# Kernel optimization log

Hardware: AMD Instinct MI355X
Metric: run time of the kernel (lower is better)

## Reference

```python
import jax, jax.numpy as jnp
import numpy as np
import math

B = 32; N = 512000; D = 64; NENT = 100000; NEDGE = 1000000; NREL = 200
K_SOURCE = 100; K_MIN = 50; K_MAX = 1000; L_INFL = 4; A_SLOPE = 1.0
TEMP = 1.0; LAM_NOISE = 1.0; COS_EPS = 1e-8


def compute_topk(l):
    # sigmoid schedule for layer-dependent Top-K (python ints, trace-time)
    if l < L_INFL:
        s = 1.0 / (1.0 + math.exp(-A_SLOPE * (l - L_INFL / 2)))
        return int(K_SOURCE + (K_MAX - K_SOURCE) * s)
    s = 1.0 / (1.0 + math.exp(-A_SLOPE * (l - 3 * L_INFL / 2)))
    return int(K_MIN + (K_MAX - K_MIN) * (1.0 - s))


def setup_inputs():
    key = jax.random.key(0)
    k = jax.random.split(key, 14)
    i = jnp.arange(N)
    b = i % B                     # batches interleaved -> every batch has diff nodes
    e = (i // B) * 6 + b          # unique entity per (batch, node), max < NENT
    nodes = jnp.stack([b, e], axis=1)
    return {
        "hidden": jax.random.normal(k[0], (N, D), jnp.float32),
        "nodes": nodes,
        "scores": jax.random.uniform(k[1], (N,), jnp.float32) + 0.1,
        "h0": jax.random.normal(k[2], (1, N, D), jnp.float32),
        "alpha": jax.random.normal(k[3], (NEDGE, 1), jnp.float32),
        "hidden_q": jax.random.normal(k[4], (B, D), jnp.float32),
        "q_rel": jax.random.randint(k[5], (B,), 0, 2 * NREL + 1),
        "edges": jax.random.randint(k[6], (NEDGE, 6), 0, N),
        "old_nodes_new_idx": jnp.arange(N // 2),
        "batch_size": B,
        "message": jax.random.normal(k[7], (NEDGE, D), jnp.float32),
        "obj": jax.random.randint(k[8], (NEDGE,), 0, N),
        "alpha_temp": jax.random.normal(k[9], (NEDGE, 1), jnp.float32),
        "l": 2,
        "noise": jax.random.normal(k[10], (N, 3), jnp.float32),
        "mlp_w1": jax.random.normal(k[11], (2 * D, D), jnp.float32) * 0.05,
        "mlp_b1": jnp.zeros((D,), jnp.float32),
        "mlp_w2": jax.random.normal(k[12], (D, D), jnp.float32) * 0.05,
        "mlp_b2": jnp.zeros((D,), jnp.float32),
        "rel_embed": jax.random.normal(k[13], (2 * NREL + 1, D), jnp.float32) * 0.05,
        "expert_emb": jax.random.normal(jax.random.fold_in(key, 1), (3, D), jnp.float32),
        "w_n": jax.random.normal(jax.random.fold_in(key, 2), (D,), jnp.float32) * 0.05,
    }


def _dense_topk_mult(vals, bidx, eidx, diff, K, B_):
    # scatter per-diff-node values into dense [B, n_ent], softmax over entities,
    # top-K hard mask, straight-through multiplier (hard - sg(p) + p) on diff nodes.
    neg = jnp.float32(-jnp.inf)
    dense = jnp.full((B_, NENT), neg, jnp.float32).at[bidx, eidx].set(jnp.where(diff, vals, neg))
    probs = jax.nn.softmax(dense, axis=1)
    _, idx = jax.lax.top_k(probs, K)
    hard = jnp.zeros((B_, NENT), bool).at[jnp.arange(B_)[:, None], idx].set(True)
    p = probs[bidx, eidx]
    h = hard[bidx, eidx].astype(jnp.float32)
    return jnp.where(diff, h - jax.lax.stop_gradient(p) + p, 1.0)


def _forward(hidden, scores, h0, hidden_q, alpha_temp, mlp_w1, mlp_b1, mlp_w2, mlp_b2,
             rel_embed, expert_emb, w_n, nodes, q_rel, edges, old_nodes_new_idx,
             batch_size, noise, l):
    bidx = nodes[:, 0]
    eidx = nodes[:, 1]
    # ---- noisy gate over 3 pruning experts ----
    q_rel_e = rel_embed[q_rel]                                   # [B, D]
    ctx_in = jnp.concatenate([hidden_q[bidx], q_rel_e[bidx]], axis=-1)  # [N, 2D]
    ctx = jax.nn.relu(ctx_in @ mlp_w1 + mlp_b1) @ mlp_w2 + mlp_b2       # [N, D]
    escore = ctx @ expert_emb.T                                  # [N, 3]
    nscale = jax.nn.softplus(ctx @ w_n)[:, None]                 # [N, 1]
    escore = escore + LAM_NOISE * noise * nscale
    weights = jax.nn.softmax(escore / TEMP, axis=-1)             # [N, 3]
    importance = weights.sum(0) / weights.sum()                  # [3], sums to 1
    w = importance  # num_pruning_experts=3: topk over all 3 + renorm is identity

    diff = jnp.ones((N,), bool).at[old_nodes_new_idx].set(False)
    K_l = compute_topk(l)

    # expert 0: score-based pruner
    m0 = _dense_topk_mult(scores, bidx, eidx, diff, K_l, batch_size)

    # expert 1: cosine-similarity pruner (hidden vs query relation embedding)
    qn = q_rel_e[bidx]
    num = (hidden * qn).sum(-1)
    den = jnp.maximum(jnp.linalg.norm(hidden, axis=-1), COS_EPS) * \
          jnp.maximum(jnp.linalg.norm(qn, axis=-1), COS_EPS)
    m1 = _dense_topk_mult(num / den, bidx, eidx, diff, K_l, batch_size)

    # expert 2: alpha pruner -- segment-max of edge attention onto target nodes,
    # softmax over the global node dim, top-K among new nodes only.
    obj_e = edges[:, 5]
    mx = jax.ops.segment_max(alpha_temp[:, 0], obj_e, num_segments=N)
    node_probs = jax.nn.softmax(mx / TEMP)
    masked = jnp.where(diff, node_probs, -1.0)   # probs >= 0, so topk lands on diff
    _, top_i = jax.lax.top_k(masked, K_l)
    hard2 = jnp.zeros((N,), bool).at[top_i].set(True)
    m2 = jnp.where(diff, hard2.astype(jnp.float32) - jax.lax.stop_gradient(node_probs) + node_probs, 1.0)

    # ---- combine: each expert returns the full node set with diff rows rescaled,
    # and the hashed node-id lookup is the identity permutation here, so the
    # index_add combine reduces to a weighted sum of multipliers. ----
    wm = w[0] * m0 + w[1] * m1 + w[2] * m2                        # [N]
    hidden_c = hidden * wm[:, None]
    scores_c = scores * wm
    h0_c = h0 * wm[None, :, None]

    cv = jnp.std(weights, ddof=1) / (weights.mean() + 1e-5)       # torch unbiased std
    L_imp = cv ** 2
    return hidden_c, scores_c, h0_c, L_imp


def reference(hidden, nodes, scores, h0, alpha, hidden_q, q_rel, edges,
              old_nodes_new_idx, batch_size, message, obj, alpha_temp, l, noise,
              mlp_w1, mlp_b1, mlp_w2, mlp_b2, rel_embed, expert_emb, w_n):
    # alpha / message / obj are passed through in the original but unused in the
    # computed path; the final scores!=0 row filter is replaced by keeping the
    # full (zero-preserving) arrays to stay jit-compatible.
    return _forward(hidden, scores, h0, hidden_q, alpha_temp, mlp_w1, mlp_b1,
                    mlp_w2, mlp_b2, rel_embed, expert_emb, w_n, nodes, q_rel,
                    edges, old_nodes_new_idx, batch_size, noise, l)
```

## Files before the change

kernel.cpp:

```cpp
#include <hip/hip_runtime.h>
#include <stdint.h>
#include <math.h>

#define DD 64
#define K_SOURCE_C 100
#define K_MIN_C 50
#define K_MAX_C 1000
#define L_INFL_C 4
#define A_SLOPE_C 1.0
#define COS_EPS_C 1e-8f
#define NSEL_MAX 65
#define NBINS 8192

__device__ __forceinline__ uint32_t f2mono(float f) {
    uint32_t u = __float_as_uint(f);
    return (u & 0x80000000u) ? ~u : (u | 0x80000000u);
}

__constant__ int c_shifts[5] = {51, 38, 25, 12, 0};
__constant__ int c_nbits[5]  = {13, 13, 13, 13, 12};

__global__ void init_kernel(uint32_t* mx, uint8_t* diff, int* cnt, double* sums,
                            int* Kp, const int* l_ptr, int N, int B) {
    int i = blockIdx.x * blockDim.x + threadIdx.x;
    if (i < N) { mx[i] = 0u; diff[i] = 1; }
    if (i < B) cnt[i] = 0;
    if (i < 4) sums[i] = 0.0;
    if (i == 0) {
        double l = (double)(*l_ptr);
        int K;
        if (l < (double)L_INFL_C) {
            double s = 1.0 / (1.0 + exp(-A_SLOPE_C * (l - L_INFL_C / 2.0)));
            K = (int)(K_SOURCE_C + (K_MAX_C - K_SOURCE_C) * s);
        } else {
            double s = 1.0 / (1.0 + exp(-A_SLOPE_C * (l - 3.0 * L_INFL_C / 2.0)));
            K = (int)(K_MIN_C + (K_MAX_C - K_MIN_C) * (1.0 - s));
        }
        *Kp = K;
    }
}

__global__ void zero_ghist_kernel(uint32_t* ghist, int total) {
    int i = blockIdx.x * blockDim.x + threadIdx.x;
    if (i < total) ghist[i] = 0;
}

__global__ void state_init_kernel(uint64_t* prefix, uint32_t* Krs, uint32_t* done,
                                  const int* Kp, int nsel) {
    int s = threadIdx.x;
    if (s < nsel) { prefix[s] = 0ull; Krs[s] = (uint32_t)(*Kp); done[s] = 0u; }
}

__global__ void diff_kernel(uint8_t* diff, const int* old_idx, int n_old, int N) {
    int j = blockIdx.x * blockDim.x + threadIdx.x;
    if (j < n_old) { int idx = old_idx[j]; if (idx >= 0 && idx < N) diff[idx] = 0; }
}

__global__ void ctx_kernel(const float* hidden_q, const int* q_rel, const float* rel_embed,
                           const float* w1, const float* b1, const float* w2, const float* b2,
                           const float* expert_emb, const float* w_n,
                           float* escore, float* nscale, float* qvec, float* qnorm, int B) {
    int b = blockIdx.x, t = threadIdx.x;
    __shared__ float cin[2 * DD];
    __shared__ float h1s[DD];
    int q = q_rel[b];
    float qv = rel_embed[(size_t)q * DD + t];
    qvec[b * DD + t] = qv;
    cin[t] = hidden_q[b * DD + t];
    cin[DD + t] = qv;
    __syncthreads();
    float acc = b1[t];
    for (int j = 0; j < 2 * DD; j++) acc += cin[j] * w1[j * DD + t];
    h1s[t] = fmaxf(acc, 0.f);
    __syncthreads();
    float c = b2[t];
    for (int j = 0; j < DD; j++) c += h1s[j] * w2[j * DD + t];
    float e0 = c * expert_emb[0 * DD + t];
    float e1 = c * expert_emb[1 * DD + t];
    float e2 = c * expert_emb[2 * DD + t];
    float wn = c * w_n[t];
    float qq = qv * qv;
    for (int m = 32; m >= 1; m >>= 1) {
        e0 += __shfl_xor(e0, m); e1 += __shfl_xor(e1, m); e2 += __shfl_xor(e2, m);
        wn += __shfl_xor(wn, m); qq += __shfl_xor(qq, m);
    }
    if (t == 0) {
        escore[b * 3 + 0] = e0; escore[b * 3 + 1] = e1; escore[b * 3 + 2] = e2;
        nscale[b] = fmaxf(wn, 0.f) + log1pf(expf(-fabsf(wn)));
        qnorm[b] = fmaxf(sqrtf(qq), COS_EPS_C);
    }
}

__global__ void weights_kernel(const int* nodes, const float* noise, const float* escore,
                               const float* nscale, double* sums, int N, int B) {
    int i = blockIdx.x * blockDim.x + threadIdx.x;
    double s0 = 0, s1 = 0, s2 = 0, sq = 0;
    if (i < N) {
        int b = nodes[2 * i];
        if (b >= 0 && b < B) {
            float ns = nscale[b];
            float e0 = escore[b * 3 + 0] + noise[3 * i + 0] * ns;
            float e1 = escore[b * 3 + 1] + noise[3 * i + 1] * ns;
            float e2 = escore[b * 3 + 2] + noise[3 * i + 2] * ns;
            float m = fmaxf(e0, fmaxf(e1, e2));
            float x0 = expf(e0 - m), x1 = expf(e1 - m), x2 = expf(e2 - m);
            float s = x0 + x1 + x2;
            x0 /= s; x1 /= s; x2 /= s;
            s0 = x0; s1 = x1; s2 = x2;
            sq = (double)x0 * x0 + (double)x1 * x1 + (double)x2 * x2;
        }
    }
    for (int m = 32; m >= 1; m >>= 1) {
        s0 += __shfl_xor(s0, m); s1 += __shfl_xor(s1, m);
        s2 += __shfl_xor(s2, m); sq += __shfl_xor(sq, m);
    }
    __shared__ double red[4][4];
    int wid = threadIdx.x >> 6, lane = threadIdx.x & 63;
    if (lane == 0) { red[wid][0] = s0; red[wid][1] = s1; red[wid][2] = s2; red[wid][3] = sq; }
    __syncthreads();
    if (threadIdx.x == 0) {
        int nw = blockDim.x >> 6;
        double a0 = 0, a1 = 0, a2 = 0, a3 = 0;
        for (int w = 0; w < nw; w++) { a0 += red[w][0]; a1 += red[w][1]; a2 += red[w][2]; a3 += red[w][3]; }
        atomicAdd(&sums[0], a0); atomicAdd(&sums[1], a1);
        atomicAdd(&sums[2], a2); atomicAdd(&sums[3], a3);
    }
}

__global__ void stats_kernel(const double* sums, float* wvec, float* out_L, int N) {
    double c0 = sums[0], c1 = sums[1], c2 = sums[2], S2 = sums[3];
    double tot = c0 + c1 + c2;
    wvec[0] = (float)(c0 / tot); wvec[1] = (float)(c1 / tot); wvec[2] = (float)(c2 / tot);
    double n = 3.0 * (double)N;
    double mean = tot / n;
    double var = (S2 - tot * tot / n) / (n - 1.0);
    if (var < 0) var = 0;
    double cv = sqrt(var) / (mean + 1e-5);
    *out_L = (float)(cv * cv);
}

__global__ void cos_kernel(const float* hidden, const int* nodes, const float* qvec,
                           const float* qnorm, float* cosvals, int N, int B) {
    int t = threadIdx.x;
    int node = blockIdx.x * 16 + (t >> 4);
    int sub = t & 15;
    if (node >= N) return;
    int b = nodes[2 * node];
    float4 h4 = *(const float4*)(hidden + (size_t)node * DD + sub * 4);
    float num = 0.f;
    if (b >= 0 && b < B) {
        float4 q4 = *(const float4*)(qvec + b * DD + sub * 4);
        num = h4.x * q4.x + h4.y * q4.y + h4.z * q4.z + h4.w * q4.w;
    }
    float hs = h4.x * h4.x + h4.y * h4.y + h4.z * h4.z + h4.w * h4.w;
    for (int m = 8; m >= 1; m >>= 1) { num += __shfl_xor(num, m); hs += __shfl_xor(hs, m); }
    if (sub == 0) {
        float qn = (b >= 0 && b < B) ? qnorm[b] : COS_EPS_C;
        cosvals[node] = num / (fmaxf(sqrtf(hs), COS_EPS_C) * qn);
    }
}

__global__ void segmax_kernel(const int* edges, const float* alpha_temp, uint32_t* mx,
                              int NE, int N) {
    int e = blockIdx.x * blockDim.x + threadIdx.x;
    if (e < NE) {
        int o = edges[(size_t)e * 6 + 5];
        if (o >= 0 && o < N) atomicMax(&mx[o], f2mono(alpha_temp[e]));
    }
}

__global__ void compact_kernel(const int* nodes, const uint8_t* diff, const float* scores,
                               const float* cosvals, uint64_t* keys0, uint64_t* keys1,
                               int* cnt, int N, int B, int CAP) {
    __shared__ int lcnt[64];
    __shared__ int lbase[64];
    int t = threadIdx.x;
    if (t < B) lcnt[t] = 0;
    __syncthreads();
    int i = blockIdx.x * blockDim.x + t;
    int b = -1, loc = 0;
    if (i < N && diff[i]) {
        int bb = nodes[2 * i];
        if (bb >= 0 && bb < B) { b = bb; loc = atomicAdd(&lcnt[b], 1); }
    }
    __syncthreads();
    if (t < B) lbase[t] = lcnt[t] ? atomicAdd(&cnt[t], lcnt[t]) : 0;
    __syncthreads();
    if (b >= 0) {
        int pos = lbase[b] + loc;
        if (pos < CAP) {
            int ei = nodes[2 * i + 1];
            uint64_t tb = (uint64_t)(0xFFFFFFFFu - (uint32_t)ei);
            keys0[(size_t)b * CAP + pos] = ((uint64_t)f2mono(scores[i]) << 32) | tb;
            keys1[(size_t)b * CAP + pos] = ((uint64_t)f2mono(cosvals[i]) << 32) | tb;
        }
    }
}

__global__ __launch_bounds__(1024)
void hist_kernel(const uint64_t* keys0, const uint64_t* keys1, const int* cnt,
                 const uint8_t* diff, const uint32_t* mx,
                 const uint64_t* prefix, const uint32_t* done,
                 uint32_t* ghist, int lev, int N, int B, int CAP) {
    int sel = blockIdx.y;
    if (done[sel]) return;
    __shared__ uint32_t hist[NBINS];
    int t = threadIdx.x;
    for (int j = t; j < NBINS; j += 1024) hist[j] = 0;
    __syncthreads();
    uint64_t pmask = (lev == 0) ? 0ull : (~0ull << c_shifts[lev - 1]);
    uint64_t pref = prefix[sel];
    int sh = c_shifts[lev];
    uint32_t bmask = (1u << c_nbits[lev]) - 1u;
    int stride = gridDim.x * 1024;
    int base = blockIdx.x * 1024 + t;
    if (sel < 2 * B) {
        int row = (sel < B) ? sel : sel - B;
        const uint64_t* list = ((sel < B) ? keys0 : keys1) + (size_t)row * CAP;
        int n = min(cnt[row], CAP);
        for (int i = base; i < n; i += stride) {
            uint64_t key = list[i];
            if ((key & pmask) == pref)
                atomicAdd(&hist[(uint32_t)(key >> sh) & bmask], 1u);
        }
    } else {
        for (int i = base; i < N; i += stride) {
            if (diff[i]) {
                uint64_t key = ((uint64_t)mx[i] << 32) | (uint64_t)(0xFFFFFFFFu - (uint32_t)i);
                if ((key & pmask) == pref)
                    atomicAdd(&hist[(uint32_t)(key >> sh) & bmask], 1u);
            }
        }
    }
    __syncthreads();
    uint32_t* g = ghist + (size_t)sel * NBINS;
    for (int j = t; j < NBINS; j += 1024) {
        uint32_t v = hist[j];
        if (v) atomicAdd(&g[j], v);
    }
}

__global__ __launch_bounds__(1024)
void pick_kernel(uint32_t* ghist, uint64_t* prefix, uint32_t* Krs, uint32_t* done,
                 uint64_t* T, int lev, int B) {
    int sel = blockIdx.x;
    if (done[sel]) return;
    __shared__ uint32_t hist[NBINS];
    __shared__ uint32_t wtot[16];
    __shared__ uint64_t sh_prefix;
    __shared__ uint32_t sh_K;
    __shared__ int sh_found;
    int t = threadIdx.x;
    uint32_t* g = ghist + (size_t)sel * NBINS;
    uint32_t csum = 0;
#pragma unroll
    for (int j = 0; j < 8; j++) {
        uint32_t v = g[8 * t + j];
        hist[8 * t + j] = v;
        g[8 * t + j] = 0;
        csum += v;
    }
    uint32_t ssum = csum;
    int lane = t & 63, wid = t >> 6;
#pragma unroll
    for (int off = 1; off < 64; off <<= 1) {
        uint32_t v = __shfl_down(ssum, off, 64);
        if (lane + off < 64) ssum += v;
    }
    if (lane == 0) wtot[wid] = ssum;
    if (t == 0) sh_found = 0;
    __syncthreads();
    uint32_t above_waves = 0, total = 0;
#pragma unroll
    for (int w = 0; w < 16; w++) {
        uint32_t v = wtot[w];
        total += v;
        if (w > wid) above_waves += v;
    }
    uint32_t suffix_incl = ssum + above_waves;
    uint32_t Kr = Krs[sel];
    uint64_t pref = prefix[sel];
    int sh = c_shifts[lev];
    if (lev == 0 && total <= Kr) {
        if (t == 0) { T[sel] = 0ull; done[sel] = 1u; }
        return;
    }
    uint32_t gcnt = suffix_incl - csum;
    int fd = -1; uint32_t fK = 0;
#pragma unroll
    for (int j = 7; j >= 0; j--) {
        uint32_t h = hist[8 * t + j];
        if (gcnt < Kr && gcnt + h >= Kr) { fd = 8 * t + j; fK = Kr - gcnt; }
        gcnt += h;
    }
    if (fd >= 0) { sh_prefix = pref | ((uint64_t)fd << sh); sh_K = fK; sh_found = 1; }
    __syncthreads();
    if (t == 0) {
        if (sh_found) {
            if (lev == 4) { T[sel] = sh_prefix; done[sel] = 1u; }
            else { prefix[sel] = sh_prefix; Krs[sel] = sh_K; }
        } else {
            T[sel] = 0ull; done[sel] = 1u;
        }
    }
}

__global__ void final_kernel(const float* hidden, const float* h0, const float* scores,
                             const int* nodes, const uint8_t* diff, const float* cosvals,
                             const uint32_t* mx, const uint64_t* T, const float* wvec,
                             float* out_hidden, float* out_scores, float* out_h0,
                             int N, int B) {
    int t = threadIdx.x;
    int node = blockIdx.x * 16 + (t >> 4);
    int sub = t & 15;
    if (node >= N) return;
    float w0 = wvec[0], w1 = wvec[1], w2 = wvec[2];
    float wm;
    if (!diff[node]) {
        wm = w0 + w1 + w2;
    } else {
        int b = nodes[2 * node];
        int ei = nodes[2 * node + 1];
        float m0 = 0.f, m1 = 0.f;
        if (b >= 0 && b < B) {
            uint64_t tb = (uint64_t)(0xFFFFFFFFu - (uint32_t)ei);
            uint64_t k0 = ((uint64_t)f2mono(scores[node]) << 32) | tb;
            uint64_t k1 = ((uint64_t)f2mono(cosvals[node]) << 32) | tb;
            m0 = (k0 >= T[b]) ? 1.f : 0.f;
            m1 = (k1 >= T[B + b]) ? 1.f : 0.f;
        }
        uint64_t k2 = ((uint64_t)mx[node] << 32) | (uint64_t)(0xFFFFFFFFu - (uint32_t)node);
        float m2 = (k2 >= T[2 * B]) ? 1.f : 0.f;
        wm = w0 * m0 + w1 * m1 + w2 * m2;
    }
    size_t off = (size_t)node * DD + sub * 4;
    float4 h4 = *(const float4*)(hidden + off);
    float4 g4 = *(const float4*)(h0 + off);
    float4 o1, o2;
    o1.x = h4.x * wm; o1.y = h4.y * wm; o1.z = h4.z * wm; o1.w = h4.w * wm;
    o2.x = g4.x * wm; o2.y = g4.y * wm; o2.z = g4.z * wm; o2.w = g4.w * wm;
    *(float4*)(out_hidden + off) = o1;
    *(float4*)(out_h0 + off) = o2;
    if (sub == 0) out_scores[node] = scores[node] * wm;
}

extern "C" void kernel_launch(void* const* d_in, const int* in_sizes, int n_in,
                              void* d_out, int out_size, void* d_ws, size_t ws_size,
                              hipStream_t stream) {
    const float* hidden     = (const float*)d_in[0];
    const int*   nodes      = (const int*)d_in[1];
    const float* scores     = (const float*)d_in[2];
    const float* h0         = (const float*)d_in[3];
    const float* hidden_q   = (const float*)d_in[5];
    const int*   q_rel      = (const int*)d_in[6];
    const int*   edges      = (const int*)d_in[7];
    const int*   old_idx    = (const int*)d_in[8];
    const float* alpha_temp = (const float*)d_in[12];
    const int*   l_ptr      = (const int*)d_in[13];
    const float* noise      = (const float*)d_in[14];
    const float* mw1        = (const float*)d_in[15];
    const float* mb1        = (const float*)d_in[16];
    const float* mw2        = (const float*)d_in[17];
    const float* mb2        = (const float*)d_in[18];
    const float* rel_embed  = (const float*)d_in[19];
    const float* expert_emb = (const float*)d_in[20];
    const float* w_n        = (const float*)d_in[21];

    int N     = in_sizes[2];
    int NE    = in_sizes[12];
    int n_old = in_sizes[8];
    int B     = in_sizes[5] / DD;
    int CAP   = N / B;
    int nsel  = 2 * B + 1;

    size_t off = 0;
    auto take = [&](size_t bytes) -> size_t {
        size_t p = off; off += (bytes + 15) & ~(size_t)15; return p;
    };
    char* wsb = (char*)d_ws;
    float*    cosvals = (float*)   (wsb + take((size_t)N * 4));
    uint32_t* mx      = (uint32_t*)(wsb + take((size_t)N * 4));
    uint8_t*  diff    = (uint8_t*) (wsb + take((size_t)N));
    int*      cnt     = (int*)     (wsb + take((size_t)B * 4));
    double*   sums    = (double*)  (wsb + take(4 * 8));
    int*      Kp      = (int*)     (wsb + take(16));
    float*    escore  = (float*)   (wsb + take((size_t)B * 3 * 4));
    float*    nscale  = (float*)   (wsb + take((size_t)B * 4));
    float*    qvec    = (float*)   (wsb + take((size_t)B * DD * 4));
    float*    qnorm   = (float*)   (wsb + take((size_t)B * 4));
    float*    wvec    = (float*)   (wsb + take(16));
    uint64_t* T       = (uint64_t*)(wsb + take((size_t)nsel * 8));
    uint64_t* prefix  = (uint64_t*)(wsb + take((size_t)nsel * 8));
    uint32_t* Krs     = (uint32_t*)(wsb + take((size_t)nsel * 4));
    uint32_t* done    = (uint32_t*)(wsb + take((size_t)nsel * 4));
    uint32_t* ghist   = (uint32_t*)(wsb + take((size_t)nsel * NBINS * 4));
    size_t keys_bytes = (size_t)B * CAP * 8;
    uint64_t *keys0, *keys1;
    if (ws_size >= off + 2 * keys_bytes) {
        keys0 = (uint64_t*)(wsb + take(keys_bytes));
        keys1 = (uint64_t*)(wsb + take(keys_bytes));
    } else {
        keys0 = (uint64_t*)d_out;
        keys1 = keys0 + (size_t)B * CAP;
    }

    float* out_hidden = (float*)d_out;
    float* out_scores = out_hidden + (size_t)N * DD;
    float* out_h0     = out_scores + N;
    float* out_L      = out_h0 + (size_t)N * DD;

    int nb = (N + 255) / 256;
    init_kernel<<<nb, 256, 0, stream>>>(mx, diff, cnt, sums, Kp, l_ptr, N, B);
    zero_ghist_kernel<<<(nsel * NBINS + 1023) / 1024, 1024, 0, stream>>>(ghist, nsel * NBINS);
    state_init_kernel<<<1, 128, 0, stream>>>(prefix, Krs, done, Kp, nsel);
    diff_kernel<<<(n_old + 255) / 256, 256, 0, stream>>>(diff, old_idx, n_old, N);
    ctx_kernel<<<B, 64, 0, stream>>>(hidden_q, q_rel, rel_embed, mw1, mb1, mw2, mb2,
                                     expert_emb, w_n, escore, nscale, qvec, qnorm, B);
    weights_kernel<<<nb, 256, 0, stream>>>(nodes, noise, escore, nscale, sums, N, B);
    stats_kernel<<<1, 1, 0, stream>>>(sums, wvec, out_L, N);
    cos_kernel<<<(N + 15) / 16, 256, 0, stream>>>(hidden, nodes, qvec, qnorm, cosvals, N, B);
    segmax_kernel<<<(NE + 255) / 256, 256, 0, stream>>>(edges, alpha_temp, mx, NE, N);
    compact_kernel<<<nb, 256, 0, stream>>>(nodes, diff, scores, cosvals, keys0, keys1, cnt, N, B, CAP);
    dim3 hgrid(64, nsel);
    for (int lev = 0; lev < 5; lev++) {
        hist_kernel<<<hgrid, 1024, 0, stream>>>(keys0, keys1, cnt, diff, mx,
                                                prefix, done, ghist, lev, N, B, CAP);
        pick_kernel<<<nsel, 1024, 0, stream>>>(ghist, prefix, Krs, done, T, lev, B);
    }
    final_kernel<<<(N + 15) / 16, 256, 0, stream>>>(hidden, h0, scores, nodes, diff, cosvals,
                                                    mx, T, wvec, out_hidden, out_scores, out_h0, N, B);
}
```

Before: 872.1 us.

## Fuse radix-select levels into per-block kernels and merge cosine with weights pass

Replaces the 5-level multi-kernel radix select (10 launches over a 65-row global histogram) with selA, which runs all five levels for each per-batch list inside one block, plus a global-node selection path. That path builds a level-0 histogram over compacted node keys, then gathers candidates into LDS in selB for the remaining levels. The cosine and expert-weight kernels are fused so hidden rows and nodes are read in one pass, and ghist and state init are folded into the init kernel. This removes many launches and repeated full scans over N. The risk is that the single-block selB becomes a serial bottleneck when the candidate set overflows LDS.

```diff
diff --git a/kernel.cpp b/kernel.cpp
--- a/kernel.cpp
+++ b/kernel.cpp
@@ -9,8 +9,9 @@
 #define L_INFL_C 4
 #define A_SLOPE_C 1.0
 #define COS_EPS_C 1e-8f
-#define NSEL_MAX 65
 #define NBINS 8192
+#define CAPC 3584
+#define NHB 192
 
 __device__ __forceinline__ uint32_t f2mono(float f) {
     uint32_t u = __float_as_uint(f);
@@ -21,12 +22,15 @@
 __constant__ int c_nbits[5]  = {13, 13, 13, 13, 12};
 
 __global__ void init_kernel(uint32_t* mx, uint8_t* diff, int* cnt, double* sums,
-                            int* Kp, const int* l_ptr, int N, int B) {
+                            int* Kp, int* node_cnt, uint32_t* ghist,
+                            const int* l_ptr, int N, int B) {
     int i = blockIdx.x * blockDim.x + threadIdx.x;
     if (i < N) { mx[i] = 0u; diff[i] = 1; }
     if (i < B) cnt[i] = 0;
     if (i < 4) sums[i] = 0.0;
+    if (i < NBINS) ghist[i] = 0u;
     if (i == 0) {
+        *node_cnt = 0;
         double l = (double)(*l_ptr);
         int K;
         if (l < (double)L_INFL_C) {
@@ -38,17 +42,6 @@
         }
         *Kp = K;
     }
-}
-
-__global__ void zero_ghist_kernel(uint32_t* ghist, int total) {
-    int i = blockIdx.x * blockDim.x + threadIdx.x;
-    if (i < total) ghist[i] = 0;
-}
-
-__global__ void state_init_kernel(uint64_t* prefix, uint32_t* Krs, uint32_t* done,
-                                  const int* Kp, int nsel) {
-    int s = threadIdx.x;
-    if (s < nsel) { prefix[s] = 0ull; Krs[s] = (uint32_t)(*Kp); done[s] = 0u; }
 }
 
 __global__ void diff_kernel(uint8_t* diff, const int* old_idx, int n_old, int N) {
@@ -91,23 +84,49 @@
     }
 }
 
-__global__ void weights_kernel(const int* nodes, const float* noise, const float* escore,
-                               const float* nscale, double* sums, int N, int B) {
-    int i = blockIdx.x * blockDim.x + threadIdx.x;
+__global__ void segmax_kernel(const int* edges, const float* alpha_temp, uint32_t* mx,
+                              int NE, int N) {
+    int e = blockIdx.x * blockDim.x + threadIdx.x;
+    if (e < NE) {
+        int o = edges[(size_t)e * 6 + 5];
+        if (o >= 0 && o < N) atomicMax(&mx[o], f2mono(alpha_temp[e]));
+    }
+}
+
+__global__ void nodewc_kernel(const float* hidden, const int* nodes, const float* noise,
+                              const float* qvec, const float* qnorm,
+                              const float* escore, const float* nscale,
+                              float* cosvals, double* sums, int N, int B) {
+    int t = threadIdx.x;
+    int node = blockIdx.x * 16 + (t >> 4);
+    int sub = t & 15;
     double s0 = 0, s1 = 0, s2 = 0, sq = 0;
-    if (i < N) {
-        int b = nodes[2 * i];
-        if (b >= 0 && b < B) {
-            float ns = nscale[b];
-            float e0 = escore[b * 3 + 0] + noise[3 * i + 0] * ns;
-            float e1 = escore[b * 3 + 1] + noise[3 * i + 1] * ns;
-            float e2 = escore[b * 3 + 2] + noise[3 * i + 2] * ns;
-            float m = fmaxf(e0, fmaxf(e1, e2));
-            float x0 = expf(e0 - m), x1 = expf(e1 - m), x2 = expf(e2 - m);
-            float s = x0 + x1 + x2;
-            x0 /= s; x1 /= s; x2 /= s;
-            s0 = x0; s1 = x1; s2 = x2;
-            sq = (double)x0 * x0 + (double)x1 * x1 + (double)x2 * x2;
+    if (node < N) {
+        int b = nodes[2 * node];
+        bool bv = (b >= 0 && b < B);
+        float4 h4 = *(const float4*)(hidden + (size_t)node * DD + sub * 4);
+        float num = 0.f;
+        if (bv) {
+            float4 q4 = *(const float4*)(qvec + b * DD + sub * 4);
+            num = h4.x * q4.x + h4.y * q4.y + h4.z * q4.z + h4.w * q4.w;
+        }
+        float hs = h4.x * h4.x + h4.y * h4.y + h4.z * h4.z + h4.w * h4.w;
+        for (int m = 8; m >= 1; m >>= 1) { num += __shfl_xor(num, m); hs += __shfl_xor(hs, m); }
+        if (sub == 0) {
+            float qn = bv ? qnorm[b] : COS_EPS_C;
+            cosvals[node] = num / (fmaxf(sqrtf(hs), COS_EPS_C) * qn);
+            if (bv) {
+                float ns = nscale[b];
+                float e0 = escore[b * 3 + 0] + noise[3 * node + 0] * ns;
+                float e1 = escore[b * 3 + 1] + noise[3 * node + 1] * ns;
+                float e2 = escore[b * 3 + 2] + noise[3 * node + 2] * ns;
+                float mm = fmaxf(e0, fmaxf(e1, e2));
+                float x0 = expf(e0 - mm), x1 = expf(e1 - mm), x2 = expf(e2 - mm);
+                float s = x0 + x1 + x2;
+                x0 /= s; x1 /= s; x2 /= s;
+                s0 = x0; s1 = x1; s2 = x2;
+                sq = (double)x0 * x0 + (double)x1 * x1 + (double)x2 * x2;
+            }
         }
     }
     for (int m = 32; m >= 1; m >>= 1) {
@@ -115,13 +134,12 @@
         s2 += __shfl_xor(s2, m); sq += __shfl_xor(sq, m);
     }
     __shared__ double red[4][4];
-    int wid = threadIdx.x >> 6, lane = threadIdx.x & 63;
+    int wid = t >> 6, lane = t & 63;
     if (lane == 0) { red[wid][0] = s0; red[wid][1] = s1; red[wid][2] = s2; red[wid][3] = sq; }
     __syncthreads();
-    if (threadIdx.x == 0) {
-        int nw = blockDim.x >> 6;
+    if (t == 0) {
         double a0 = 0, a1 = 0, a2 = 0, a3 = 0;
-        for (int w = 0; w < nw; w++) { a0 += red[w][0]; a1 += red[w][1]; a2 += red[w][2]; a3 += red[w][3]; }
+        for (int w = 0; w < 4; w++) { a0 += red[w][0]; a1 += red[w][1]; a2 += red[w][2]; a3 += red[w][3]; }
         atomicAdd(&sums[0], a0); atomicAdd(&sums[1], a1);
         atomicAdd(&sums[2], a2); atomicAdd(&sums[3], a3);
     }
@@ -139,170 +157,178 @@
     *out_L = (float)(cv * cv);
 }
 
-__global__ void cos_kernel(const float* hidden, const int* nodes, const float* qvec,
-                           const float* qnorm, float* cosvals, int N, int B) {
-    int t = threadIdx.x;
-    int node = blockIdx.x * 16 + (t >> 4);
-    int sub = t & 15;
-    if (node >= N) return;
-    int b = nodes[2 * node];
-    float4 h4 = *(const float4*)(hidden + (size_t)node * DD + sub * 4);
-    float num = 0.f;
-    if (b >= 0 && b < B) {
-        float4 q4 = *(const float4*)(qvec + b * DD + sub * 4);
-        num = h4.x * q4.x + h4.y * q4.y + h4.z * q4.z + h4.w * q4.w;
-    }
-    float hs = h4.x * h4.x + h4.y * h4.y + h4.z * h4.z + h4.w * h4.w;
-    for (int m = 8; m >= 1; m >>= 1) { num += __shfl_xor(num, m); hs += __shfl_xor(hs, m); }
-    if (sub == 0) {
-        float qn = (b >= 0 && b < B) ? qnorm[b] : COS_EPS_C;
-        cosvals[node] = num / (fmaxf(sqrtf(hs), COS_EPS_C) * qn);
-    }
-}
-
-__global__ void segmax_kernel(const int* edges, const float* alpha_temp, uint32_t* mx,
-                              int NE, int N) {
-    int e = blockIdx.x * blockDim.x + threadIdx.x;
-    if (e < NE) {
-        int o = edges[(size_t)e * 6 + 5];
-        if (o >= 0 && o < N) atomicMax(&mx[o], f2mono(alpha_temp[e]));
-    }
-}
-
 __global__ void compact_kernel(const int* nodes, const uint8_t* diff, const float* scores,
-                               const float* cosvals, uint64_t* keys0, uint64_t* keys1,
-                               int* cnt, int N, int B, int CAP) {
+                               const float* cosvals, const uint32_t* mx,
+                               uint64_t* keys0, uint64_t* keys1, uint64_t* nkeys,
+                               int* cnt, int* node_cnt, int N, int B, int CAP) {
     __shared__ int lcnt[64];
     __shared__ int lbase[64];
+    __shared__ int nloc_cnt, nloc_base;
     int t = threadIdx.x;
     if (t < B) lcnt[t] = 0;
+    if (t == 0) nloc_cnt = 0;
     __syncthreads();
     int i = blockIdx.x * blockDim.x + t;
-    int b = -1, loc = 0;
-    if (i < N && diff[i]) {
+    int b = -1, loc = 0, nl = 0;
+    bool isdiff = (i < N) && diff[i];
+    if (isdiff) {
+        nl = atomicAdd(&nloc_cnt, 1);
         int bb = nodes[2 * i];
         if (bb >= 0 && bb < B) { b = bb; loc = atomicAdd(&lcnt[b], 1); }
     }
     __syncthreads();
     if (t < B) lbase[t] = lcnt[t] ? atomicAdd(&cnt[t], lcnt[t]) : 0;
-    __syncthreads();
-    if (b >= 0) {
-        int pos = lbase[b] + loc;
-        if (pos < CAP) {
-            int ei = nodes[2 * i + 1];
-            uint64_t tb = (uint64_t)(0xFFFFFFFFu - (uint32_t)ei);
-            keys0[(size_t)b * CAP + pos] = ((uint64_t)f2mono(scores[i]) << 32) | tb;
-            keys1[(size_t)b * CAP + pos] = ((uint64_t)f2mono(cosvals[i]) << 32) | tb;
-        }
-    }
+    if (t == 0) nloc_base = nloc_cnt ? atomicAdd(node_cnt, nloc_cnt) : 0;
+    __syncthreads();
+    if (isdiff) {
+        nkeys[nloc_base + nl] = ((uint64_t)mx[i] << 32) | (uint64_t)(0xFFFFFFFFu - (uint32_t)i);
+        if (b >= 0) {
+            int pos = lbase[b] + loc;
+            if (pos < CAP) {
+                int ei = nodes[2 * i + 1];
+                uint64_t tb = (uint64_t)(0xFFFFFFFFu - (uint32_t)ei);
+                keys0[(size_t)b * CAP + pos] = ((uint64_t)f2mono(scores[i]) << 32) | tb;
+                keys1[(size_t)b * CAP + pos] = ((uint64_t)f2mono(cosvals[i]) << 32) | tb;
+            }
+        }
+    }
+}
+
+struct PickScratch { uint32_t wtot[16]; int fd; uint32_t fK; uint32_t total; };
+
+__device__ void block_pick(const uint32_t* hist, int nbins, uint32_t Kr, PickScratch* sc) {
+    int t = threadIdx.x;
+    int PB = nbins >> 10;
+    int lane = t & 63, wid = t >> 6;
+    uint32_t csum = 0;
+    for (int j = 0; j < PB; j++) csum += hist[PB * t + j];
+    uint32_t ssum = csum;
+    for (int off = 1; off < 64; off <<= 1) {
+        uint32_t v = __shfl_down(ssum, off, 64);
+        if (lane + off < 64) ssum += v;
+    }
+    if (lane == 0) sc->wtot[wid] = ssum;
+    if (t == 0) sc->fd = -1;
+    __syncthreads();
+    uint32_t above = 0, total = 0;
+    for (int w = 0; w < 16; w++) {
+        uint32_t v = sc->wtot[w];
+        total += v;
+        if (w > wid) above += v;
+    }
+    uint32_t gcnt = ssum + above - csum;
+    int fd = -1; uint32_t fK = 0;
+    for (int j = PB - 1; j >= 0; j--) {
+        uint32_t h = hist[PB * t + j];
+        if (h && gcnt < Kr && gcnt + h >= Kr) { fd = PB * t + j; fK = Kr - gcnt; }
+        gcnt += h;
+    }
+    if (fd >= 0) { sc->fd = fd; sc->fK = fK; }
+    if (t == 0) sc->total = total;
+    __syncthreads();
 }
 
 __global__ __launch_bounds__(1024)
-void hist_kernel(const uint64_t* keys0, const uint64_t* keys1, const int* cnt,
-                 const uint8_t* diff, const uint32_t* mx,
-                 const uint64_t* prefix, const uint32_t* done,
-                 uint32_t* ghist, int lev, int N, int B, int CAP) {
-    int sel = blockIdx.y;
-    if (done[sel]) return;
+void selA_kernel(const uint64_t* keys0, const uint64_t* keys1, const int* cnt,
+                 const uint64_t* nkeys, const int* node_cnt, uint32_t* ghist,
+                 uint64_t* T, const int* Kp, int B, int CAP) {
     __shared__ uint32_t hist[NBINS];
-    int t = threadIdx.x;
-    for (int j = t; j < NBINS; j += 1024) hist[j] = 0;
-    __syncthreads();
-    uint64_t pmask = (lev == 0) ? 0ull : (~0ull << c_shifts[lev - 1]);
-    uint64_t pref = prefix[sel];
-    int sh = c_shifts[lev];
-    uint32_t bmask = (1u << c_nbits[lev]) - 1u;
-    int stride = gridDim.x * 1024;
-    int base = blockIdx.x * 1024 + t;
-    if (sel < 2 * B) {
-        int row = (sel < B) ? sel : sel - B;
-        const uint64_t* list = ((sel < B) ? keys0 : keys1) + (size_t)row * CAP;
+    __shared__ PickScratch sc;
+    int t = threadIdx.x;
+    int blk = blockIdx.x;
+    if (blk < 2 * B) {
+        int row = (blk < B) ? blk : blk - B;
+        const uint64_t* list = ((blk < B) ? keys0 : keys1) + (size_t)row * CAP;
         int n = min(cnt[row], CAP);
-        for (int i = base; i < n; i += stride) {
-            uint64_t key = list[i];
-            if ((key & pmask) == pref)
-                atomicAdd(&hist[(uint32_t)(key >> sh) & bmask], 1u);
-        }
-    } else {
-        for (int i = base; i < N; i += stride) {
-            if (diff[i]) {
-                uint64_t key = ((uint64_t)mx[i] << 32) | (uint64_t)(0xFFFFFFFFu - (uint32_t)i);
+        int K = *Kp;
+        if (n <= K) { if (t == 0) T[blk] = 0ull; return; }
+        uint64_t pref = 0ull;
+        uint32_t Kr = (uint32_t)K;
+        for (int lev = 0; lev < 5; lev++) {
+            int nb = 1 << c_nbits[lev];
+            for (int j = t; j < nb; j += 1024) hist[j] = 0;
+            __syncthreads();
+            uint64_t pmask = (lev == 0) ? 0ull : (~0ull << c_shifts[lev - 1]);
+            int sh = c_shifts[lev];
+            uint32_t bmask = (uint32_t)(nb - 1);
+            for (int i = t; i < n; i += 1024) {
+                uint64_t key = list[i];
                 if ((key & pmask) == pref)
                     atomicAdd(&hist[(uint32_t)(key >> sh) & bmask], 1u);
             }
-        }
-    }
-    __syncthreads();
-    uint32_t* g = ghist + (size_t)sel * NBINS;
-    for (int j = t; j < NBINS; j += 1024) {
-        uint32_t v = hist[j];
-        if (v) atomicAdd(&g[j], v);
+            __syncthreads();
+            block_pick(hist, nb, Kr, &sc);
+            if (sc.fd < 0) { if (t == 0) T[blk] = 0ull; return; }
+            pref |= ((uint64_t)sc.fd) << sh;
+            Kr = sc.fK;
+            __syncthreads();
+        }
+        if (t == 0) T[blk] = pref;
+    } else {
+        int nb = blk - 2 * B;
+        for (int j = t; j < NBINS; j += 1024) hist[j] = 0;
+        __syncthreads();
+        int n = *node_cnt;
+        for (int i = nb * 1024 + t; i < n; i += NHB * 1024)
+            atomicAdd(&hist[(uint32_t)(nkeys[i] >> 51)], 1u);
+        __syncthreads();
+        for (int j = t; j < NBINS; j += 1024) {
+            uint32_t v = hist[j];
+            if (v) atomicAdd(&ghist[j], v);
+        }
     }
 }
 
 __global__ __launch_bounds__(1024)
-void pick_kernel(uint32_t* ghist, uint64_t* prefix, uint32_t* Krs, uint32_t* done,
-                 uint64_t* T, int lev, int B) {
-    int sel = blockIdx.x;
-    if (done[sel]) return;
+void selB_kernel(const uint64_t* nkeys, const int* node_cnt, const uint32_t* ghist,
+                 uint64_t* T, const int* Kp, int B) {
     __shared__ uint32_t hist[NBINS];
-    __shared__ uint32_t wtot[16];
-    __shared__ uint64_t sh_prefix;
-    __shared__ uint32_t sh_K;
-    __shared__ int sh_found;
-    int t = threadIdx.x;
-    uint32_t* g = ghist + (size_t)sel * NBINS;
-    uint32_t csum = 0;
-#pragma unroll
-    for (int j = 0; j < 8; j++) {
-        uint32_t v = g[8 * t + j];
-        hist[8 * t + j] = v;
-        g[8 * t + j] = 0;
-        csum += v;
-    }
-    uint32_t ssum = csum;
-    int lane = t & 63, wid = t >> 6;
-#pragma unroll
-    for (int off = 1; off < 64; off <<= 1) {
-        uint32_t v = __shfl_down(ssum, off, 64);
-        if (lane + off < 64) ssum += v;
-    }
-    if (lane == 0) wtot[wid] = ssum;
-    if (t == 0) sh_found = 0;
-    __syncthreads();
-    uint32_t above_waves = 0, total = 0;
-#pragma unroll
-    for (int w = 0; w < 16; w++) {
-        uint32_t v = wtot[w];
-        total += v;
-        if (w > wid) above_waves += v;
-    }
-    uint32_t suffix_incl = ssum + above_waves;
-    uint32_t Kr = Krs[sel];
-    uint64_t pref = prefix[sel];
-    int sh = c_shifts[lev];
-    if (lev == 0 && total <= Kr) {
-        if (t == 0) { T[sel] = 0ull; done[sel] = 1u; }
-        return;
-    }
-    uint32_t gcnt = suffix_incl - csum;
-    int fd = -1; uint32_t fK = 0;
-#pragma unroll
-    for (int j = 7; j >= 0; j--) {
-        uint32_t h = hist[8 * t + j];
-        if (gcnt < Kr && gcnt + h >= Kr) { fd = 8 * t + j; fK = Kr - gcnt; }
-        gcnt += h;
-    }
-    if (fd >= 0) { sh_prefix = pref | ((uint64_t)fd << sh); sh_K = fK; sh_found = 1; }
-    __syncthreads();
-    if (t == 0) {
-        if (sh_found) {
-            if (lev == 4) { T[sel] = sh_prefix; done[sel] = 1u; }
-            else { prefix[sel] = sh_prefix; Krs[sel] = sh_K; }
-        } else {
-            T[sel] = 0ull; done[sel] = 1u;
-        }
-    }
+    __shared__ uint64_t cand[CAPC];
+    __shared__ PickScratch sc;
+    __shared__ int ccnt;
+    int t = threadIdx.x;
+    int K = *Kp;
+    int n = *node_cnt;
+    for (int j = t; j < NBINS; j += 1024) hist[j] = ghist[j];
+    __syncthreads();
+    block_pick(hist, NBINS, (uint32_t)K, &sc);
+    if (sc.total <= (uint32_t)K || sc.fd < 0) { if (t == 0) T[2 * B] = 0ull; return; }
+    int fd0 = sc.fd;
+    uint64_t pref = ((uint64_t)fd0) << 51;
+    uint32_t Kr = sc.fK;
+    if (t == 0) ccnt = 0;
+    __syncthreads();
+    for (int i = t; i < n; i += 1024) {
+        uint64_t key = nkeys[i];
+        if ((int)(key >> 51) == fd0) {
+            int p = atomicAdd(&ccnt, 1);
+            if (p < CAPC) cand[p] = key;
+        }
+    }
+    __syncthreads();
+    int m = ccnt;
+    bool inlds = (m <= CAPC);
+    if (!inlds) m = n;
+    for (int lev = 1; lev < 5; lev++) {
+        int nb = 1 << c_nbits[lev];
+        for (int j = t; j < nb; j += 1024) hist[j] = 0;
+        __syncthreads();
+        uint64_t pmask = ~0ull << c_shifts[lev - 1];
+        int sh = c_shifts[lev];
+        uint32_t bmask = (uint32_t)(nb - 1);
+        for (int i = t; i < m; i += 1024) {
+            uint64_t key = inlds ? cand[i] : nkeys[i];
+            if ((key & pmask) == pref)
+                atomicAdd(&hist[(uint32_t)(key >> sh) & bmask], 1u);
+        }
+        __syncthreads();
+        block_pick(hist, nb, Kr, &sc);
+        if (sc.fd < 0) { if (t == 0) T[2 * B] = 0ull; return; }
+        pref |= ((uint64_t)sc.fd) << sh;
+        Kr = sc.fK;
+        __syncthreads();
+    }
+    if (t == 0) T[2 * B] = pref;
 }
 
 __global__ void final_kernel(const float* hidden, const float* h0, const float* scores,
@@ -378,30 +404,31 @@
         size_t p = off; off += (bytes + 15) & ~(size_t)15; return p;
     };
     char* wsb = (char*)d_ws;
-    float*    cosvals = (float*)   (wsb + take((size_t)N * 4));
-    uint32_t* mx      = (uint32_t*)(wsb + take((size_t)N * 4));
-    uint8_t*  diff    = (uint8_t*) (wsb + take((size_t)N));
-    int*      cnt     = (int*)     (wsb + take((size_t)B * 4));
-    double*   sums    = (double*)  (wsb + take(4 * 8));
-    int*      Kp      = (int*)     (wsb + take(16));
-    float*    escore  = (float*)   (wsb + take((size_t)B * 3 * 4));
-    float*    nscale  = (float*)   (wsb + take((size_t)B * 4));
-    float*    qvec    = (float*)   (wsb + take((size_t)B * DD * 4));
-    float*    qnorm   = (float*)   (wsb + take((size_t)B * 4));
-    float*    wvec    = (float*)   (wsb + take(16));
-    uint64_t* T       = (uint64_t*)(wsb + take((size_t)nsel * 8));
-    uint64_t* prefix  = (uint64_t*)(wsb + take((size_t)nsel * 8));
-    uint32_t* Krs     = (uint32_t*)(wsb + take((size_t)nsel * 4));
-    uint32_t* done    = (uint32_t*)(wsb + take((size_t)nsel * 4));
-    uint32_t* ghist   = (uint32_t*)(wsb + take((size_t)nsel * NBINS * 4));
-    size_t keys_bytes = (size_t)B * CAP * 8;
-    uint64_t *keys0, *keys1;
-    if (ws_size >= off + 2 * keys_bytes) {
+    float*    cosvals  = (float*)   (wsb + take((size_t)N * 4));
+    uint32_t* mx       = (uint32_t*)(wsb + take((size_t)N * 4));
+    uint8_t*  diff     = (uint8_t*) (wsb + take((size_t)N));
+    int*      cnt      = (int*)     (wsb + take((size_t)B * 4));
+    double*   sums     = (double*)  (wsb + take(4 * 8));
+    int*      Kp       = (int*)     (wsb + take(16));
+    int*      node_cnt = (int*)     (wsb + take(16));
+    float*    escore   = (float*)   (wsb + take((size_t)B * 3 * 4));
+    float*    nscale   = (float*)   (wsb + take((size_t)B * 4));
+    float*    qvec     = (float*)   (wsb + take((size_t)B * DD * 4));
+    float*    qnorm    = (float*)   (wsb + take((size_t)B * 4));
+    float*    wvec     = (float*)   (wsb + take(16));
+    uint64_t* T        = (uint64_t*)(wsb + take((size_t)nsel * 8));
+    uint32_t* ghist    = (uint32_t*)(wsb + take((size_t)NBINS * 4));
+    size_t keys_bytes  = (size_t)B * CAP * 8;
+    size_t nkeys_bytes = (size_t)N * 8;
+    uint64_t *keys0, *keys1, *nkeys;
+    if (ws_size >= off + 2 * keys_bytes + nkeys_bytes) {
         keys0 = (uint64_t*)(wsb + take(keys_bytes));
         keys1 = (uint64_t*)(wsb + take(keys_bytes));
+        nkeys = (uint64_t*)(wsb + take(nkeys_bytes));
     } else {
         keys0 = (uint64_t*)d_out;
         keys1 = keys0 + (size_t)B * CAP;
+        nkeys = keys1 + (size_t)B * CAP;
     }
 
     float* out_hidden = (float*)d_out;
@@ -410,23 +437,19 @@
     float* out_L      = out_h0 + (size_t)N * DD;
 
     int nb = (N + 255) / 256;
-    init_kernel<<<nb, 256, 0, stream>>>(mx, diff, cnt, sums, Kp, l_ptr, N, B);
-    zero_ghist_kernel<<<(nsel * NBINS + 1023) / 1024, 1024, 0, stream>>>(ghist, nsel * NBINS);
-    state_init_kernel<<<1, 128, 0, stream>>>(prefix, Krs, done, Kp, nsel);
+    init_kernel<<<nb, 256, 0, stream>>>(mx, diff, cnt, sums, Kp, node_cnt, ghist, l_ptr, N, B);
     diff_kernel<<<(n_old + 255) / 256, 256, 0, stream>>>(diff, old_idx, n_old, N);
     ctx_kernel<<<B, 64, 0, stream>>>(hidden_q, q_rel, rel_embed, mw1, mb1, mw2, mb2,
                                      expert_emb, w_n, escore, nscale, qvec, qnorm, B);
-    weights_kernel<<<nb, 256, 0, stream>>>(nodes, noise, escore, nscale, sums, N, B);
+    segmax_kernel<<<(NE + 255) / 256, 256, 0, stream>>>(edges, alpha_temp, mx, NE, N);
+    nodewc_kernel<<<(N + 15) / 16, 256, 0, stream>>>(hidden, nodes, noise, qvec, qnorm,
+                                                     escore, nscale, cosvals, sums, N, B);
     stats_kernel<<<1, 1, 0, stream>>>(sums, wvec, out_L, N);
-    cos_kernel<<<(N + 15) / 16, 256, 0, stream>>>(hidden, nodes, qvec, qnorm, cosvals, N, B);
-    segmax_kernel<<<(NE + 255) / 256, 256, 0, stream>>>(edges, alpha_temp, mx, NE, N);
-    compact_kernel<<<nb, 256, 0, stream>>>(nodes, diff, scores, cosvals, keys0, keys1, cnt, N, B, CAP);
-    dim3 hgrid(64, nsel);
-    for (int lev = 0; lev < 5; lev++) {
-        hist_kernel<<<hgrid, 1024, 0, stream>>>(keys0, keys1, cnt, diff, mx,
-                                                prefix, done, ghist, lev, N, B, CAP);
-        pick_kernel<<<nsel, 1024, 0, stream>>>(ghist, prefix, Krs, done, T, lev, B);
-    }
+    compact_kernel<<<nb, 256, 0, stream>>>(nodes, diff, scores, cosvals, mx,
+                                           keys0, keys1, nkeys, cnt, node_cnt, N, B, CAP);
+    selA_kernel<<<2 * B + NHB, 1024, 0, stream>>>(keys0, keys1, cnt, nkeys, node_cnt,
+                                                  ghist, T, Kp, B, CAP);
+    selB_kernel<<<1, 1024, 0, stream>>>(nkeys, node_cnt, ghist, T, Kp, B);
     final_kernel<<<(N + 15) / 16, 256, 0, stream>>>(hidden, h0, scores, nodes, diff, cosvals,
                                                     mx, T, wvec, out_hidden, out_scores, out_h0, N, B);
 }
```

After: 2.902 ms. 3.33x slower.
